# Performance work log

Measured on AMD Instinct MI355X. Metric: run time of the kernel, lower is better.

Reference implementation:

```python
import jax, jax.numpy as jnp
import numpy as np
import math

Ds = 2048
N = 16384
M = 1024


def setup_inputs() -> dict:
    key = jax.random.key(0)
    kD, kS, kW = jax.random.split(key, 3)
    D = jax.random.normal(kD, (N, Ds), dtype=jnp.float32)
    S = jax.random.normal(kS, (M, Ds), dtype=jnp.float32)
    W = jax.random.normal(kW, (Ds, Ds), dtype=jnp.float32) * 0.01  # init.normal std=0.01
    return {"D": D, "S": S, "W": W}


def reference(D, S, W):
    ds = D.shape[1]
    temperature = 1.0
    # cross-attention: [n, m]
    scores = (D @ S.T) / (math.sqrt(ds) * temperature)
    att_weight = jax.nn.softmax(scores, axis=1)
    att_S = att_weight @ S  # [n, Ds]
    # bilinear per row: logits[i] = D[i] . (W @ att_S[i])  -> fused einsum
    logits = jnp.einsum('nd,de,ne->n', D, W, att_S)
    log_prob = jnp.sum(jax.nn.log_sigmoid(logits))
    return log_prob
```

## Files before the change

### kernel.cpp

```cpp
#include <hip/hip_runtime.h>
#include <stdint.h>

typedef unsigned short u16;
typedef unsigned int u32;
typedef __attribute__((ext_vector_type(8))) short bf16x8;
typedef __attribute__((ext_vector_type(4))) float f32x4;

#define DS 2048
#define NROWS 16384
#define MS 1024
#define K2 2048

__device__ __forceinline__ u16 f2bf(float f) {
  u32 u = __float_as_uint(f);
  u32 r = (u + 0x7fffu + ((u >> 16) & 1u)) >> 16;
  return (u16)r;
}
__device__ __forceinline__ float bf2f(u16 h) {
  return __uint_as_float(((u32)h) << 16);
}

__global__ __launch_bounds__(256) void k_conv(const float* __restrict__ in,
                                              u16* __restrict__ out, int n4) {
  int i = blockIdx.x * blockDim.x + threadIdx.x;
  int stride = gridDim.x * blockDim.x;
  for (; i < n4; i += stride) {
    float4 v = ((const float4*)in)[i];
    ushort4 o;
    o.x = f2bf(v.x); o.y = f2bf(v.y); o.z = f2bf(v.z); o.w = f2bf(v.w);
    ((ushort4*)out)[i] = o;
  }
}

__global__ __launch_bounds__(256) void k_conv_S(const float* __restrict__ in,
                                                u16* __restrict__ Sbf,
                                                u16* __restrict__ Bt, int n4) {
  int i = blockIdx.x * blockDim.x + threadIdx.x;
  int stride = gridDim.x * blockDim.x;
  for (; i < n4; i += stride) {
    float4 v = ((const float4*)in)[i];
    ushort4 o;
    o.x = f2bf(v.x); o.y = f2bf(v.y); o.z = f2bf(v.z); o.w = f2bf(v.w);
    ((ushort4*)Sbf)[i] = o;
    int m = i >> 9;
    int c4 = i & 511;
    ((ushort4*)Bt)[(size_t)m * 1024 + c4] = o;
  }
}

__device__ __forceinline__ void gload16(const u16* g, u16* l) {
  __builtin_amdgcn_global_load_lds(
      (const __attribute__((address_space(1))) void*)g,
      (__attribute__((address_space(3))) void*)l, 16, 0, 0);
}

__global__ __launch_bounds__(256, 2) void k_gemm_bt64(const u16* __restrict__ A,
                                                      const u16* __restrict__ Bt,
                                                      u16* __restrict__ C, int ldc,
                                                      int K) {
  __shared__ u16 lsA[64 * 32];
  __shared__ u16 lsB[128 * 32];
  const int tid = threadIdx.x;
  const int wid = tid >> 6;
  const int lane = tid & 63;
  const int brow = blockIdx.y * 64;
  const int bcol = blockIdx.x * 128;
  const int wm = wid >> 1;
  const int wn = wid & 1;

  f32x4 acc[2][4];
#pragma unroll
  for (int i = 0; i < 2; ++i)
#pragma unroll
    for (int j = 0; j < 4; ++j) acc[i][j] = (f32x4){0.f, 0.f, 0.f, 0.f};

  const int srow = lane >> 2;
  const int skoct = (lane & 3) * 8;
  const u16* gA = A + (size_t)(brow + wid * 16 + srow) * K + skoct;
  const u16* gB = Bt + (size_t)(bcol + wid * 32 + srow) * K + skoct;
  u16* lA = &lsA[(wid * 16) * 32];
  u16* lB0 = &lsB[(wid * 32) * 32];
  u16* lB1 = &lsB[(wid * 32 + 16) * 32];
  const size_t row16 = (size_t)16 * K;

  const int arow = wm * 32 + (lane & 15);
  const int bcr = wn * 64 + (lane & 15);
  const int koff = (lane >> 4) * 8;

  for (int kt = 0; kt < K; kt += 32) {
    gload16(gA + kt, lA);
    gload16(gB + kt, lB0);
    gload16(gB + kt + row16, lB1);
    __syncthreads();
    bf16x8 af[2], bfr[4];
#pragma unroll
    for (int i = 0; i < 2; ++i) af[i] = *(const bf16x8*)&lsA[(arow + i * 16) * 32 + koff];
#pragma unroll
    for (int i = 0; i < 4; ++i) bfr[i] = *(const bf16x8*)&lsB[(bcr + i * 16) * 32 + koff];
#pragma unroll
    for (int mi = 0; mi < 2; ++mi)
#pragma unroll
      for (int ni = 0; ni < 4; ++ni)
        acc[mi][ni] = __builtin_amdgcn_mfma_f32_16x16x32_bf16(af[mi], bfr[ni],
                                                              acc[mi][ni], 0, 0, 0);
    __syncthreads();
  }

  const int crow0 = brow + wm * 32 + (lane >> 4) * 4;
  const int ccol0 = bcol + wn * 64 + (lane & 15);
#pragma unroll
  for (int mi = 0; mi < 2; ++mi)
#pragma unroll
    for (int ni = 0; ni < 4; ++ni)
#pragma unroll
      for (int r = 0; r < 4; ++r)
        C[(size_t)(crow0 + mi * 16 + r) * ldc + (ccol0 + ni * 16)] = f2bf(acc[mi][ni][r]);
}

#define SINV 0.022097086912079608f

#define DSR(d, a, IMM) \
  asm volatile("ds_read_b128 %0, %1 offset:%c2" : "=v"(d) : "v"(a), "n"(IMM))

#define RD_A0(k0, k1, dst)                              \
  DSR(dst[0][0], k0, 0);     DSR(dst[0][1], k1, 0);     \
  DSR(dst[1][0], k0, 2048);  DSR(dst[1][1], k1, 2048);  \
  DSR(dst[2][0], k0, 4096);  DSR(dst[2][1], k1, 4096);  \
  DSR(dst[3][0], k0, 6144);  DSR(dst[3][1], k1, 6144)
#define RD_A1(k0, k1, dst)                              \
  DSR(dst[0][0], k0, 16384); DSR(dst[0][1], k1, 16384); \
  DSR(dst[1][0], k0, 18432); DSR(dst[1][1], k1, 18432); \
  DSR(dst[2][0], k0, 20480); DSR(dst[2][1], k1, 20480); \
  DSR(dst[3][0], k0, 22528); DSR(dst[3][1], k1, 22528)
#define RD_B0(k0, k1, dst)                              \
  DSR(dst[0][0], k0, 0);     DSR(dst[0][1], k1, 0);     \
  DSR(dst[1][0], k0, 2048);  DSR(dst[1][1], k1, 2048)
#define RD_B1(k0, k1, dst)                              \
  DSR(dst[0][0], k0, 16384); DSR(dst[0][1], k1, 16384); \
  DSR(dst[1][0], k0, 18432); DSR(dst[1][1], k1, 18432)

#define MMAQ(AF, BQ, QM, QN)                                                       \
  do {                                                                             \
    _Pragma("unroll") for (int mi = 0; mi < 4; ++mi)                               \
        _Pragma("unroll") for (int ni = 0; ni < 2; ++ni) {                         \
      acc[QM][QN][mi][ni] = __builtin_amdgcn_mfma_f32_16x16x32_bf16(               \
          AF[mi][0], BQ[ni][0], acc[QM][QN][mi][ni], 0, 0, 0);                     \
      acc[QM][QN][mi][ni] = __builtin_amdgcn_mfma_f32_16x16x32_bf16(               \
          AF[mi][1], BQ[ni][1], acc[QM][QN][mi][ni], 0, 0, 0);                     \
    }                                                                              \
  } while (0)

#define LGKM(N)                                              \
  asm volatile("s_waitcnt lgkmcnt(" #N ")" ::: "memory");    \
  __builtin_amdgcn_sched_barrier(0)
#define VMW(N) asm volatile("s_waitcnt vmcnt(" #N ")" ::: "memory")
#define PRIO1() __builtin_amdgcn_s_setprio(1)
#define PRIO0() __builtin_amdgcn_s_setprio(0)
#define BAR() __builtin_amdgcn_s_barrier()

#define STGA(b, h, kt)                                                            \
  do {                                                                            \
    gload16(pA + (size_t)((h) * 128) * K2 + (kt),                                 \
            &lds[(b) * 32768 + (h) * 8192 + wid * 512]);                          \
    gload16(pA + (size_t)((h) * 128 + 64) * K2 + (kt),                            \
            &lds[(b) * 32768 + (h) * 8192 + 4096 + wid * 512]);                   \
  } while (0)
#define STGB(b, h, kt)                                                            \
  do {                                                                            \
    gload16(pB + (size_t)((h) * 128) * K2 + (kt),                                 \
            &lds[(b) * 32768 + 16384 + (h) * 8192 + wid * 512]);                  \
    gload16(pB + (size_t)((h) * 128 + 64) * K2 + (kt),                            \
            &lds[(b) * 32768 + 16384 + (h) * 8192 + 4096 + wid * 512]);           \
  } while (0)

__global__ __launch_bounds__(512, 2) void k_gemm8(const u16* __restrict__ A,
                                                  const u16* __restrict__ Bt,
                                                  float* __restrict__ Pnd) {
  extern __shared__ u16 lds[];
  const int tid = threadIdx.x;
  const int wid = tid >> 6;
  const int lane = tid & 63;
  const int bid = blockIdx.x;
  const int swz = (bid & 7) * 64 + (bid >> 3);
  const int by = swz >> 3, bx = swz & 7;
  const int brow = by * 256, bcol = bx * 256;
  const int wm = wid >> 2, wn = wid & 3;
  const int l15 = lane & 15, s0 = lane >> 4;

  const int tr = tid >> 3;
  const int scol = ((tid & 7) ^ (tr & 7)) << 3;
  const u16* pA = A + (size_t)(brow + tr) * K2 + scol;
  const u16* pB = Bt + (size_t)(bcol + tr) * K2 + scol;

  const u32 lb = (u32)(uintptr_t)(&lds[0]);
  const u32 xorp = ((u32)(s0 ^ (lane & 7))) << 4;
  const u32 aA00 = lb + ((u32)(wm * 64 + l15) << 7) + xorp;
  const u32 aA01 = aA00 ^ 64u;
  const u32 aA10 = aA00 + 65536u;
  const u32 aA11 = aA10 ^ 64u;
  const u32 aB00 = lb + 32768u + ((u32)(wn * 32 + l15) << 7) + xorp;
  const u32 aB01 = aB00 ^ 64u;
  const u32 aB10 = aB00 + 65536u;
  const u32 aB11 = aB10 ^ 64u;

  f32x4 acc[2][2][4][2];
#pragma unroll
  for (int a = 0; a < 2; ++a)
#pragma unroll
    for (int b = 0; b < 2; ++b)
#pragma unroll
      for (int c = 0; c < 4; ++c)
#pragma unroll
        for (int d = 0; d < 2; ++d) acc[a][b][c][d] = (f32x4){0.f, 0.f, 0.f, 0.f};

  bf16x8 afA[4][2], afB[4][2], bq0[2][2], bq1[2][2];

  STGA(0, 0, 0); STGB(0, 0, 0); STGB(0, 1, 0); STGA(0, 1, 0);
  STGA(1, 0, 64);
  VMW(2);
  BAR();
  RD_A0(aA00, aA01, afA);
  RD_B0(aB00, aB01, bq0);

  int kb = 0;
#pragma unroll 1
  for (int j = 0; j < 15; ++j, kb += 128) {
    STGB(1, 0, kb + 64);
    RD_B1(aB00, aB01, bq1);
    LGKM(4); PRIO1(); MMAQ(afA, bq0, 0, 0); PRIO0(); VMW(4); BAR();
    STGB(1, 1, kb + 64);
    RD_A1(aA00, aA01, afB);
    LGKM(8); PRIO1(); MMAQ(afA, bq1, 0, 1); PRIO0(); VMW(4); BAR();
    STGA(1, 1, kb + 64);
    LGKM(0); PRIO1(); MMAQ(afB, bq0, 1, 0); PRIO0(); VMW(4); BAR();
    STGA(0, 0, kb + 128);
    RD_A0(aA10, aA11, afA);
    RD_B0(aB10, aB11, bq0);
    LGKM(12); PRIO1(); MMAQ(afB, bq1, 1, 1); PRIO0(); VMW(4); BAR();
    STGB(0, 0, kb + 128);
    RD_B1(aB10, aB11, bq1);
    LGKM(4); PRIO1(); MMAQ(afA, bq0, 0, 0); PRIO0(); VMW(4); BAR();
    STGB(0, 1, kb + 128);
    RD_A1(aA10, aA11, afB);
    LGKM(8); PRIO1(); MMAQ(afA, bq1, 0, 1); PRIO0(); VMW(4); BAR();
    STGA(0, 1, kb + 128);
    LGKM(0); PRIO1(); MMAQ(afB, bq0, 1, 0); PRIO0(); VMW(4); BAR();
    STGA(1, 0, kb + 192);
    RD_A0(aA00, aA01, afA);
    RD_B0(aB00, aB01, bq0);
    LGKM(12); PRIO1(); MMAQ(afB, bq1, 1, 1); PRIO0(); VMW(4); BAR();
  }
  {
    STGB(1, 0, kb + 64);
    RD_B1(aB00, aB01, bq1);
    LGKM(4); PRIO1(); MMAQ(afA, bq0, 0, 0); PRIO0(); VMW(4); BAR();
    STGB(1, 1, kb + 64);
    RD_A1(aA00, aA01, afB);
    LGKM(8); PRIO1(); MMAQ(afA, bq1, 0, 1); PRIO0(); VMW(4); BAR();
    STGA(1, 1, kb + 64);
    LGKM(0); PRIO1(); MMAQ(afB, bq0, 1, 0); PRIO0(); VMW(4); BAR();
    RD_A0(aA10, aA11, afA);
    RD_B0(aB10, aB11, bq0);
    LGKM(12); PRIO1(); MMAQ(afB, bq1, 1, 1); PRIO0(); VMW(2); BAR();
    RD_B1(aB10, aB11, bq1);
    LGKM(4); PRIO1(); MMAQ(afA, bq0, 0, 0); PRIO0(); VMW(0); BAR();
    RD_A1(aA10, aA11, afB);
    LGKM(8); PRIO1(); MMAQ(afA, bq1, 0, 1); PRIO0();
    LGKM(0); PRIO1(); MMAQ(afB, bq0, 1, 0); PRIO0();
    MMAQ(afB, bq1, 1, 1);
  }

  __syncthreads();
  float* red = (float*)&lds[0];

#pragma unroll
  for (int qm = 0; qm < 2; ++qm)
#pragma unroll
    for (int mi = 0; mi < 4; ++mi)
#pragma unroll
      for (int r = 0; r < 4; ++r) {
        float num = 0.f, den = 0.f;
#pragma unroll
        for (int qn = 0; qn < 2; ++qn)
#pragma unroll
          for (int ni = 0; ni < 2; ++ni) {
            float v = acc[qm][qn][mi][ni][r];
            float g = __shfl_xor(v, 1);
            float e = __expf(v * SINV);
            num += e * g;
            den += e;
          }
        num += __shfl_xor(num, 2); den += __shfl_xor(den, 2);
        num += __shfl_xor(num, 4); den += __shfl_xor(den, 4);
        num += __shfl_xor(num, 8); den += __shfl_xor(den, 8);
        if (l15 == 0) {
          int slot = qm * 16 + mi * 4 + r;
          red[((wid * 32 + slot) * 4 + s0) * 2 + 0] = num;
          red[((wid * 32 + slot) * 4 + s0) * 2 + 1] = den;
        }
      }
  __syncthreads();
  {
    int rloc = tid >> 1, which = tid & 1;
    int qm = rloc >> 7, wmr = (rloc >> 6) & 1, mi = (rloc >> 4) & 3;
    int lg = (rloc >> 2) & 3, r = rloc & 3;
    int slot = qm * 16 + mi * 4 + r;
    float v = 0.f;
#pragma unroll
    for (int w2 = 0; w2 < 4; ++w2)
      v += red[(((wmr * 4 + w2) * 32 + slot) * 4 + lg) * 2 + which];
    Pnd[((size_t)(brow + rloc) * 8 + bx) * 2 + which] = v;
  }
}

__global__ __launch_bounds__(256) void k_rowfinal(const float* __restrict__ Pnd,
                                                  float* __restrict__ part) {
  int row = blockIdx.x * 256 + threadIdx.x;
  const float4* p = (const float4*)(Pnd + (size_t)row * 16);
  float num = 0.f, den = 0.f;
#pragma unroll
  for (int i = 0; i < 4; ++i) {
    float4 v = p[i];
    num += v.x + v.z;
    den += v.y + v.w;
  }
  float logit = num / den;
  float ls = (logit >= 0.f) ? -log1pf(__expf(-logit))
                            : (logit - log1pf(__expf(logit)));
  __shared__ float red[4];
#pragma unroll
  for (int off = 32; off > 0; off >>= 1) ls += __shfl_down(ls, off);
  if ((threadIdx.x & 63) == 0) red[threadIdx.x >> 6] = ls;
  __syncthreads();
  if (threadIdx.x == 0) part[blockIdx.x] = red[0] + red[1] + red[2] + red[3];
}

__global__ __launch_bounds__(64) void k_final64(const float* __restrict__ part,
                                                float* __restrict__ out) {
  float v = part[threadIdx.x];
#pragma unroll
  for (int off = 32; off > 0; off >>= 1) v += __shfl_down(v, off);
  if (threadIdx.x == 0) out[0] = v;
}

extern "C" void kernel_launch(void* const* d_in, const int* in_sizes, int n_in,
                              void* d_out, int out_size, void* d_ws, size_t ws_size,
                              hipStream_t stream) {
  const float* D = (const float*)d_in[0];
  const float* S = (const float*)d_in[1];
  const float* W = (const float*)d_in[2];

  char* w = (char*)d_ws;
  u16* Dbf = (u16*)w; w += (size_t)NROWS * DS * 2;
  u16* Bt = (u16*)w;  w += (size_t)DS * DS * 2;
  u16* Wbf = (u16*)w; w += (size_t)DS * DS * 2;
  u16* Sbf = (u16*)w; w += (size_t)MS * DS * 2;
  float* Pnd = (float*)w; w += (size_t)NROWS * 16 * 4;
  float* part = (float*)w;

  (void)hipFuncSetAttribute((const void*)k_gemm8,
                            hipFuncAttributeMaxDynamicSharedMemorySize, 131072);

  k_conv<<<1024, 256, 0, stream>>>(W, Wbf, DS * DS / 4);
  k_conv_S<<<512, 256, 0, stream>>>(S, Sbf, Bt, MS * DS / 4);
  k_conv<<<2048, 256, 0, stream>>>(D, Dbf, NROWS * DS / 4);

  k_gemm_bt64<<<dim3(DS / 128, MS / 64), 256, 0, stream>>>(
      Sbf, Wbf, Bt + DS, 2 * DS, DS);

  k_gemm8<<<512, 512, 131072, stream>>>(Dbf, Bt, Pnd);

  k_rowfinal<<<NROWS / 256, 256, 0, stream>>>(Pnd, part);
  k_final64<<<1, 64, 0, stream>>>(part, (float*)d_out);
}
```

Baseline: 188.7 us.

## Restructure GEMM main loop into four phases with merged MFMA groups

```diff
diff --git a/kernel.cpp b/kernel.cpp
--- a/kernel.cpp
+++ b/kernel.cpp
@@ -154,6 +154,7 @@
   asm volatile("s_waitcnt lgkmcnt(" #N ")" ::: "memory");    \
   __builtin_amdgcn_sched_barrier(0)
 #define VMW(N) asm volatile("s_waitcnt vmcnt(" #N ")" ::: "memory")
+#define SB0() __builtin_amdgcn_sched_barrier(0)
 #define PRIO1() __builtin_amdgcn_s_setprio(1)
 #define PRIO0() __builtin_amdgcn_s_setprio(0)
 #define BAR() __builtin_amdgcn_s_barrier()
@@ -172,6 +173,7 @@
     gload16(pB + (size_t)((h) * 128 + 64) * K2 + (kt),                            \
             &lds[(b) * 32768 + 16384 + (h) * 8192 + 4096 + wid * 512]);           \
   } while (0)
+#define STGB4(b, kt) do { STGB(b, 0, kt); STGB(b, 1, kt); } while (0)
 
 __global__ __launch_bounds__(512, 2) void k_gemm8(const u16* __restrict__ A,
                                                   const u16* __restrict__ Bt,
@@ -215,59 +217,71 @@
 
   bf16x8 afA[4][2], afB[4][2], bq0[2][2], bq1[2][2];
 
-  STGA(0, 0, 0); STGB(0, 0, 0); STGB(0, 1, 0); STGA(0, 1, 0);
+  STGA(0, 0, 0); STGA(0, 1, 0); STGB4(0, 0);
   STGA(1, 0, 64);
   VMW(2);
   BAR();
   RD_A0(aA00, aA01, afA);
   RD_B0(aB00, aB01, bq0);
+  RD_B1(aB00, aB01, bq1);
+  STGB4(1, 64);
 
   int kb = 0;
 #pragma unroll 1
   for (int j = 0; j < 15; ++j, kb += 128) {
-    STGB(1, 0, kb + 64);
+    RD_A1(aA00, aA01, afB);
+    LGKM(8);
+    PRIO1(); MMAQ(afA, bq0, 0, 0); MMAQ(afA, bq1, 0, 1); PRIO0();
+    SB0();
+    STGA(1, 1, kb + 64);
+    STGA(0, 0, kb + 128);
+    VMW(4); BAR();
+    RD_A0(aA10, aA11, afA);
+    LGKM(8);
+    PRIO1(); MMAQ(afB, bq0, 1, 0); MMAQ(afB, bq1, 1, 1); PRIO0();
+    SB0();
+    RD_B0(aB10, aB11, bq0);
+    RD_B1(aB10, aB11, bq1);
+    STGB4(0, kb + 128);
+    VMW(4); BAR();
+    RD_A1(aA10, aA11, afB);
+    LGKM(8);
+    PRIO1(); MMAQ(afA, bq0, 0, 0); MMAQ(afA, bq1, 0, 1); PRIO0();
+    SB0();
+    STGA(0, 1, kb + 128);
+    STGA(1, 0, kb + 192);
+    VMW(4); BAR();
+    RD_A0(aA00, aA01, afA);
+    LGKM(8);
+    PRIO1(); MMAQ(afB, bq0, 1, 0); MMAQ(afB, bq1, 1, 1); PRIO0();
+    SB0();
+    RD_B0(aB00, aB01, bq0);
     RD_B1(aB00, aB01, bq1);
-    LGKM(4); PRIO1(); MMAQ(afA, bq0, 0, 0); PRIO0(); VMW(4); BAR();
-    STGB(1, 1, kb + 64);
+    STGB4(1, kb + 192);
+    VMW(4); BAR();
+  }
+  {
     RD_A1(aA00, aA01, afB);
-    LGKM(8); PRIO1(); MMAQ(afA, bq1, 0, 1); PRIO0(); VMW(4); BAR();
+    LGKM(8);
+    PRIO1(); MMAQ(afA, bq0, 0, 0); MMAQ(afA, bq1, 0, 1); PRIO0();
+    SB0();
     STGA(1, 1, kb + 64);
-    LGKM(0); PRIO1(); MMAQ(afB, bq0, 1, 0); PRIO0(); VMW(4); BAR();
-    STGA(0, 0, kb + 128);
+    VMW(2);
+    BAR();
     RD_A0(aA10, aA11, afA);
+    LGKM(8);
+    PRIO1(); MMAQ(afB, bq0, 1, 0); MMAQ(afB, bq1, 1, 1); PRIO0();
+    SB0();
     RD_B0(aB10, aB11, bq0);
-    LGKM(12); PRIO1(); MMAQ(afB, bq1, 1, 1); PRIO0(); VMW(4); BAR();
-    STGB(0, 0, kb + 128);
     RD_B1(aB10, aB11, bq1);
-    LGKM(4); PRIO1(); MMAQ(afA, bq0, 0, 0); PRIO0(); VMW(4); BAR();
-    STGB(0, 1, kb + 128);
+    VMW(0);
+    BAR();
     RD_A1(aA10, aA11, afB);
-    LGKM(8); PRIO1(); MMAQ(afA, bq1, 0, 1); PRIO0(); VMW(4); BAR();
-    STGA(0, 1, kb + 128);
-    LGKM(0); PRIO1(); MMAQ(afB, bq0, 1, 0); PRIO0(); VMW(4); BAR();
-    STGA(1, 0, kb + 192);
-    RD_A0(aA00, aA01, afA);
-    RD_B0(aB00, aB01, bq0);
-    LGKM(12); PRIO1(); MMAQ(afB, bq1, 1, 1); PRIO0(); VMW(4); BAR();
-  }
-  {
-    STGB(1, 0, kb + 64);
-    RD_B1(aB00, aB01, bq1);
-    LGKM(4); PRIO1(); MMAQ(afA, bq0, 0, 0); PRIO0(); VMW(4); BAR();
-    STGB(1, 1, kb + 64);
-    RD_A1(aA00, aA01, afB);
-    LGKM(8); PRIO1(); MMAQ(afA, bq1, 0, 1); PRIO0(); VMW(4); BAR();
-    STGA(1, 1, kb + 64);
-    LGKM(0); PRIO1(); MMAQ(afB, bq0, 1, 0); PRIO0(); VMW(4); BAR();
-    RD_A0(aA10, aA11, afA);
-    RD_B0(aB10, aB11, bq0);
-    LGKM(12); PRIO1(); MMAQ(afB, bq1, 1, 1); PRIO0(); VMW(2); BAR();
-    RD_B1(aB10, aB11, bq1);
-    LGKM(4); PRIO1(); MMAQ(afA, bq0, 0, 0); PRIO0(); VMW(0); BAR();
-    RD_A1(aA10, aA11, afB);
-    LGKM(8); PRIO1(); MMAQ(afA, bq1, 0, 1); PRIO0();
-    LGKM(0); PRIO1(); MMAQ(afB, bq0, 1, 0); PRIO0();
-    MMAQ(afB, bq1, 1, 1);
+    LGKM(8);
+    PRIO1(); MMAQ(afA, bq0, 0, 0); MMAQ(afA, bq1, 0, 1); PRIO0();
+    SB0();
+    LGKM(0);
+    PRIO1(); MMAQ(afB, bq0, 1, 0); MMAQ(afB, bq1, 1, 1); PRIO0();
   }
 
   __syncthreads();
```

After: 201.0 us. +6.5%, slower.

## Fuse D fp32-to-bf16 conversion into main GEMM A-tile loads

Applied to the files above, without the earlier changes.

```diff
diff --git a/kernel.cpp b/kernel.cpp
--- a/kernel.cpp
+++ b/kernel.cpp
@@ -5,6 +5,7 @@
 typedef unsigned int u32;
 typedef __attribute__((ext_vector_type(8))) short bf16x8;
 typedef __attribute__((ext_vector_type(4))) float f32x4;
+typedef __attribute__((ext_vector_type(4))) u32 u32x4;
 
 #define DS 2048
 #define NROWS 16384
@@ -121,6 +122,10 @@
 
 #define DSR(d, a, IMM) \
   asm volatile("ds_read_b128 %0, %1 offset:%c2" : "=v"(d) : "v"(a), "n"(IMM))
+#define GLD4o(d, a, IMM) \
+  asm volatile("global_load_dwordx4 %0, %1, off offset:%c2" : "=v"(d) : "v"(a), "n"(IMM))
+#define CVTPK(d, lo, hi) \
+  asm("v_cvt_pk_bf16_f32 %0, %1, %2" : "=v"(d) : "v"(lo), "v"(hi))
 
 #define RD_A0(k0, k1, dst)                              \
   DSR(dst[0][0], k0, 0);     DSR(dst[0][1], k1, 0);     \
@@ -154,17 +159,11 @@
   asm volatile("s_waitcnt lgkmcnt(" #N ")" ::: "memory");    \
   __builtin_amdgcn_sched_barrier(0)
 #define VMW(N) asm volatile("s_waitcnt vmcnt(" #N ")" ::: "memory")
+#define SB0() __builtin_amdgcn_sched_barrier(0)
 #define PRIO1() __builtin_amdgcn_s_setprio(1)
 #define PRIO0() __builtin_amdgcn_s_setprio(0)
 #define BAR() __builtin_amdgcn_s_barrier()
 
-#define STGA(b, h, kt)                                                            \
-  do {                                                                            \
-    gload16(pA + (size_t)((h) * 128) * K2 + (kt),                                 \
-            &lds[(b) * 32768 + (h) * 8192 + wid * 512]);                          \
-    gload16(pA + (size_t)((h) * 128 + 64) * K2 + (kt),                            \
-            &lds[(b) * 32768 + (h) * 8192 + 4096 + wid * 512]);                   \
-  } while (0)
 #define STGB(b, h, kt)                                                            \
   do {                                                                            \
     gload16(pB + (size_t)((h) * 128) * K2 + (kt),                                 \
@@ -173,7 +172,27 @@
             &lds[(b) * 32768 + 16384 + (h) * 8192 + 4096 + wid * 512]);           \
   } while (0)
 
-__global__ __launch_bounds__(512, 2) void k_gemm8(const u16* __restrict__ A,
+#define ALOAD(R, h, kt)                                                           \
+  do {                                                                            \
+    const float* _p0 = pAf + (size_t)((h) * 128) * 2048 + (kt);                   \
+    const float* _p1 = _p0 + (size_t)64 * 2048;                                   \
+    GLD4o(R[0], _p0, 0); GLD4o(R[1], _p0, 16);                                    \
+    GLD4o(R[2], _p1, 0); GLD4o(R[3], _p1, 16);                                    \
+  } while (0)
+#define AWRITE(R, b, h)                                                           \
+  do {                                                                            \
+    u32 c0, c1, c2, c3, c4, c5, c6, c7;                                           \
+    CVTPK(c0, R[0][0], R[0][1]); CVTPK(c1, R[0][2], R[0][3]);                     \
+    CVTPK(c2, R[1][0], R[1][1]); CVTPK(c3, R[1][2], R[1][3]);                     \
+    CVTPK(c4, R[2][0], R[2][1]); CVTPK(c5, R[2][2], R[2][3]);                     \
+    CVTPK(c6, R[3][0], R[3][1]); CVTPK(c7, R[3][2], R[3][3]);                     \
+    u32x4 Q0 = {c0, c1, c2, c3}, Q1 = {c4, c5, c6, c7};                           \
+    u32 wa = wbase + (b)*65536u + (h)*16384u;                                     \
+    asm volatile("ds_write_b128 %0, %1" ::"v"(wa), "v"(Q0));                      \
+    asm volatile("ds_write_b128 %0, %1 offset:8192" ::"v"(wa), "v"(Q1));          \
+  } while (0)
+
+__global__ __launch_bounds__(512, 2) void k_gemm8(const float* __restrict__ Af,
                                                   const u16* __restrict__ Bt,
                                                   float* __restrict__ Pnd) {
   extern __shared__ u16 lds[];
@@ -189,10 +208,11 @@
 
   const int tr = tid >> 3;
   const int scol = ((tid & 7) ^ (tr & 7)) << 3;
-  const u16* pA = A + (size_t)(brow + tr) * K2 + scol;
+  const float* pAf = Af + (size_t)(brow + tr) * 2048 + scol;
   const u16* pB = Bt + (size_t)(bcol + tr) * K2 + scol;
 
   const u32 lb = (u32)(uintptr_t)(&lds[0]);
+  const u32 wbase = lb + (u32)wid * 1024u + (u32)(lane * 16);
   const u32 xorp = ((u32)(s0 ^ (lane & 7))) << 4;
   const u32 aA00 = lb + ((u32)(wm * 64 + l15) << 7) + xorp;
   const u32 aA01 = aA00 ^ 64u;
@@ -214,10 +234,13 @@
         for (int d = 0; d < 2; ++d) acc[a][b][c][d] = (f32x4){0.f, 0.f, 0.f, 0.f};
 
   bf16x8 afA[4][2], afB[4][2], bq0[2][2], bq1[2][2];
-
-  STGA(0, 0, 0); STGB(0, 0, 0); STGB(0, 1, 0); STGA(0, 1, 0);
-  STGA(1, 0, 64);
-  VMW(2);
+  f32x4 ra0[4], ra1[4];
+
+  STGB(0, 0, 0); STGB(0, 1, 0);
+  ALOAD(ra0, 0, 0);  VMW(0); SB0(); AWRITE(ra0, 0, 0);
+  ALOAD(ra0, 1, 0);  VMW(0); SB0(); AWRITE(ra0, 0, 1);
+  ALOAD(ra0, 0, 64); VMW(0); SB0(); AWRITE(ra0, 1, 0);
+  LGKM(0);
   BAR();
   RD_A0(aA00, aA01, afA);
   RD_B0(aB00, aB01, bq0);
@@ -226,48 +249,55 @@
 #pragma unroll 1
   for (int j = 0; j < 15; ++j, kb += 128) {
     STGB(1, 0, kb + 64);
+    ALOAD(ra0, 1, kb + 64);
     RD_B1(aB00, aB01, bq1);
-    LGKM(4); PRIO1(); MMAQ(afA, bq0, 0, 0); PRIO0(); VMW(4); BAR();
+    LGKM(4); PRIO1(); MMAQ(afA, bq0, 0, 0); PRIO0(); BAR();
+    STGB(1, 1, kb + 64);
+    ALOAD(ra1, 0, kb + 128);
+    RD_A1(aA00, aA01, afB);
+    LGKM(8); PRIO1(); MMAQ(afA, bq1, 0, 1); PRIO0(); BAR();
+    LGKM(0); PRIO1(); MMAQ(afB, bq0, 1, 0); PRIO0();
+    VMW(6); SB0(); AWRITE(ra0, 1, 1); BAR();
+    VMW(0); SB0();
+    RD_A0(aA10, aA11, afA);
+    RD_B0(aB10, aB11, bq0);
+    LGKM(12); PRIO1(); MMAQ(afB, bq1, 1, 1); PRIO0();
+    AWRITE(ra1, 0, 0); BAR();
+    STGB(0, 0, kb + 128);
+    ALOAD(ra0, 1, kb + 128);
+    RD_B1(aB10, aB11, bq1);
+    LGKM(4); PRIO1(); MMAQ(afA, bq0, 0, 0); PRIO0(); BAR();
+    STGB(0, 1, kb + 128);
+    ALOAD(ra1, 0, kb + 192);
+    RD_A1(aA10, aA11, afB);
+    LGKM(8); PRIO1(); MMAQ(afA, bq1, 0, 1); PRIO0(); BAR();
+    LGKM(0); PRIO1(); MMAQ(afB, bq0, 1, 0); PRIO0();
+    VMW(6); SB0(); AWRITE(ra0, 0, 1); BAR();
+    VMW(0); SB0();
+    RD_A0(aA00, aA01, afA);
+    RD_B0(aB00, aB01, bq0);
+    LGKM(12); PRIO1(); MMAQ(afB, bq1, 1, 1); PRIO0();
+    AWRITE(ra1, 1, 0); BAR();
+  }
+  {
+    STGB(1, 0, kb + 64);
+    ALOAD(ra0, 1, kb + 64);
+    RD_B1(aB00, aB01, bq1);
+    LGKM(4); PRIO1(); MMAQ(afA, bq0, 0, 0); PRIO0(); BAR();
     STGB(1, 1, kb + 64);
     RD_A1(aA00, aA01, afB);
-    LGKM(8); PRIO1(); MMAQ(afA, bq1, 0, 1); PRIO0(); VMW(4); BAR();
-    STGA(1, 1, kb + 64);
-    LGKM(0); PRIO1(); MMAQ(afB, bq0, 1, 0); PRIO0(); VMW(4); BAR();
-    STGA(0, 0, kb + 128);
+    LGKM(8); PRIO1(); MMAQ(afA, bq1, 0, 1); PRIO0(); BAR();
+    LGKM(0); PRIO1(); MMAQ(afB, bq0, 1, 0); PRIO0();
+    VMW(2); SB0(); AWRITE(ra0, 1, 1); BAR();
+    VMW(0); SB0();
     RD_A0(aA10, aA11, afA);
     RD_B0(aB10, aB11, bq0);
-    LGKM(12); PRIO1(); MMAQ(afB, bq1, 1, 1); PRIO0(); VMW(4); BAR();
-    STGB(0, 0, kb + 128);
+    LGKM(12); PRIO1(); MMAQ(afB, bq1, 1, 1); PRIO0(); BAR();
     RD_B1(aB10, aB11, bq1);
-    LGKM(4); PRIO1(); MMAQ(afA, bq0, 0, 0); PRIO0(); VMW(4); BAR();
-    STGB(0, 1, kb + 128);
-    RD_A1(aA10, aA11, afB);
-    LGKM(8); PRIO1(); MMAQ(afA, bq1, 0, 1); PRIO0(); VMW(4); BAR();
-    STGA(0, 1, kb + 128);
-    LGKM(0); PRIO1(); MMAQ(afB, bq0, 1, 0); PRIO0(); VMW(4); BAR();
-    STGA(1, 0, kb + 192);
-    RD_A0(aA00, aA01, afA);
-    RD_B0(aB00, aB01, bq0);
-    LGKM(12); PRIO1(); MMAQ(afB, bq1, 1, 1); PRIO0(); VMW(4); BAR();
-  }
-  {
-    STGB(1, 0, kb + 64);
-    RD_B1(aB00, aB01, bq1);
-    LGKM(4); PRIO1(); MMAQ(afA, bq0, 0, 0); PRIO0(); VMW(4); BAR();
-    STGB(1, 1, kb + 64);
-    RD_A1(aA00, aA01, afB);
-    LGKM(8); PRIO1(); MMAQ(afA, bq1, 0, 1); PRIO0(); VMW(4); BAR();
-    STGA(1, 1, kb + 64);
-    LGKM(0); PRIO1(); MMAQ(afB, bq0, 1, 0); PRIO0(); VMW(4); BAR();
-    RD_A0(aA10, aA11, afA);
-    RD_B0(aB10, aB11, bq0);
-    LGKM(12); PRIO1(); MMAQ(afB, bq1, 1, 1); PRIO0(); VMW(2); BAR();
-    RD_B1(aB10, aB11, bq1);
-    LGKM(4); PRIO1(); MMAQ(afA, bq0, 0, 0); PRIO0(); VMW(0); BAR();
+    LGKM(4); PRIO1(); MMAQ(afA, bq0, 0, 0); PRIO0();
     RD_A1(aA10, aA11, afB);
     LGKM(8); PRIO1(); MMAQ(afA, bq1, 0, 1); PRIO0();
-    LGKM(0); PRIO1(); MMAQ(afB, bq0, 1, 0); PRIO0();
-    MMAQ(afB, bq1, 1, 1);
+    LGKM(0); PRIO1(); MMAQ(afB, bq0, 1, 0); MMAQ(afB, bq1, 1, 1); PRIO0();
   }
 
   __syncthreads();
@@ -351,7 +381,6 @@
   const float* W = (const float*)d_in[2];
 
   char* w = (char*)d_ws;
-  u16* Dbf = (u16*)w; w += (size_t)NROWS * DS * 2;
   u16* Bt = (u16*)w;  w += (size_t)DS * DS * 2;
   u16* Wbf = (u16*)w; w += (size_t)DS * DS * 2;
   u16* Sbf = (u16*)w; w += (size_t)MS * DS * 2;
@@ -363,12 +392,11 @@
 
   k_conv<<<1024, 256, 0, stream>>>(W, Wbf, DS * DS / 4);
   k_conv_S<<<512, 256, 0, stream>>>(S, Sbf, Bt, MS * DS / 4);
-  k_conv<<<2048, 256, 0, stream>>>(D, Dbf, NROWS * DS / 4);
 
   k_gemm_bt64<<<dim3(DS / 128, MS / 64), 256, 0, stream>>>(
       Sbf, Wbf, Bt + DS, 2 * DS, DS);
 
-  k_gemm8<<<512, 512, 131072, stream>>>(Dbf, Bt, Pnd);
+  k_gemm8<<<512, 512, 131072, stream>>>(D, Bt, Pnd);
 
   k_rowfinal<<<NROWS / 256, 256, 0, stream>>>(Pnd, part);
   k_final64<<<1, 64, 0, stream>>>(part, (float*)d_out);
```

New measurement: 350.7 us. +85.8%, slower.

## Double-buffer S·W GEMM LDS loads and merge W/S conversion kernels

Applied to the files above, without the earlier changes.

```diff
diff --git a/kernel.cpp b/kernel.cpp
--- a/kernel.cpp
+++ b/kernel.cpp
@@ -18,6 +18,31 @@
 }
 __device__ __forceinline__ float bf2f(u16 h) {
   return __uint_as_float(((u32)h) << 16);
+}
+
+#define NW4 (DS * DS / 4)
+#define NS4 (MS * DS / 4)
+__global__ __launch_bounds__(256) void k_conv_WS(const float* __restrict__ W,
+                                                 const float* __restrict__ S,
+                                                 u16* __restrict__ Wbf,
+                                                 u16* __restrict__ Sbf,
+                                                 u16* __restrict__ Bt) {
+  int i = blockIdx.x * 256 + threadIdx.x;
+  if (i < NW4) {
+    float4 v = ((const float4*)W)[i];
+    ushort4 o;
+    o.x = f2bf(v.x); o.y = f2bf(v.y); o.z = f2bf(v.z); o.w = f2bf(v.w);
+    ((ushort4*)Wbf)[i] = o;
+  } else {
+    int j = i - NW4;
+    float4 v = ((const float4*)S)[j];
+    ushort4 o;
+    o.x = f2bf(v.x); o.y = f2bf(v.y); o.z = f2bf(v.z); o.w = f2bf(v.w);
+    ((ushort4*)Sbf)[j] = o;
+    int m = j >> 9;
+    int c4 = j & 511;
+    ((ushort4*)Bt)[(size_t)m * 1024 + c4] = o;
+  }
 }
 
 __global__ __launch_bounds__(256) void k_conv(const float* __restrict__ in,
@@ -32,34 +57,23 @@
   }
 }
 
-__global__ __launch_bounds__(256) void k_conv_S(const float* __restrict__ in,
-                                                u16* __restrict__ Sbf,
-                                                u16* __restrict__ Bt, int n4) {
-  int i = blockIdx.x * blockDim.x + threadIdx.x;
-  int stride = gridDim.x * blockDim.x;
-  for (; i < n4; i += stride) {
-    float4 v = ((const float4*)in)[i];
-    ushort4 o;
-    o.x = f2bf(v.x); o.y = f2bf(v.y); o.z = f2bf(v.z); o.w = f2bf(v.w);
-    ((ushort4*)Sbf)[i] = o;
-    int m = i >> 9;
-    int c4 = i & 511;
-    ((ushort4*)Bt)[(size_t)m * 1024 + c4] = o;
-  }
-}
-
 __device__ __forceinline__ void gload16(const u16* g, u16* l) {
   __builtin_amdgcn_global_load_lds(
       (const __attribute__((address_space(1))) void*)g,
       (__attribute__((address_space(3))) void*)l, 16, 0, 0);
 }
 
+#define VMW3() asm volatile("s_waitcnt vmcnt(3)" ::: "memory")
+#define VMW0f() asm volatile("s_waitcnt vmcnt(0)" ::: "memory")
+#define RBAR() __builtin_amdgcn_s_barrier()
+#define RSB0() __builtin_amdgcn_sched_barrier(0)
+
 __global__ __launch_bounds__(256, 2) void k_gemm_bt64(const u16* __restrict__ A,
                                                       const u16* __restrict__ Bt,
                                                       u16* __restrict__ C, int ldc,
                                                       int K) {
-  __shared__ u16 lsA[64 * 32];
-  __shared__ u16 lsB[128 * 32];
+  __shared__ u16 lsA[2][64 * 32];
+  __shared__ u16 lsB[2][128 * 32];
   const int tid = threadIdx.x;
   const int wid = tid >> 6;
   const int lane = tid & 63;
@@ -78,33 +92,48 @@
   const int skoct = (lane & 3) * 8;
   const u16* gA = A + (size_t)(brow + wid * 16 + srow) * K + skoct;
   const u16* gB = Bt + (size_t)(bcol + wid * 32 + srow) * K + skoct;
-  u16* lA = &lsA[(wid * 16) * 32];
-  u16* lB0 = &lsB[(wid * 32) * 32];
-  u16* lB1 = &lsB[(wid * 32 + 16) * 32];
   const size_t row16 = (size_t)16 * K;
 
   const int arow = wm * 32 + (lane & 15);
   const int bcr = wn * 64 + (lane & 15);
   const int koff = (lane >> 4) * 8;
 
-  for (int kt = 0; kt < K; kt += 32) {
-    gload16(gA + kt, lA);
-    gload16(gB + kt, lB0);
-    gload16(gB + kt + row16, lB1);
-    __syncthreads();
+#define VSTG(b, kt)                                        \
+  do {                                                     \
+    gload16(gA + (kt), &lsA[b][(wid * 16) * 32]);          \
+    gload16(gB + (kt), &lsB[b][(wid * 32) * 32]);          \
+    gload16(gB + (kt) + row16, &lsB[b][(wid * 32 + 16) * 32]); \
+  } while (0)
+
+  VSTG(0, 0);
+  const int NT = K / 32;
+#pragma unroll 1
+  for (int t = 0; t < NT; ++t) {
+    const int b = t & 1;
+    if (t < NT - 1) {
+      VSTG(b ^ 1, (t + 1) * 32);
+      VMW3();
+    } else {
+      VMW0f();
+    }
+    RBAR(); RSB0();
     bf16x8 af[2], bfr[4];
 #pragma unroll
-    for (int i = 0; i < 2; ++i) af[i] = *(const bf16x8*)&lsA[(arow + i * 16) * 32 + koff];
-#pragma unroll
-    for (int i = 0; i < 4; ++i) bfr[i] = *(const bf16x8*)&lsB[(bcr + i * 16) * 32 + koff];
+    for (int i = 0; i < 2; ++i)
+      af[i] = *(const bf16x8*)&lsA[b][(arow + i * 16) * 32 + koff];
+#pragma unroll
+    for (int i = 0; i < 4; ++i)
+      bfr[i] = *(const bf16x8*)&lsB[b][(bcr + i * 16) * 32 + koff];
 #pragma unroll
     for (int mi = 0; mi < 2; ++mi)
 #pragma unroll
       for (int ni = 0; ni < 4; ++ni)
         acc[mi][ni] = __builtin_amdgcn_mfma_f32_16x16x32_bf16(af[mi], bfr[ni],
                                                               acc[mi][ni], 0, 0, 0);
-    __syncthreads();
-  }
+    RSB0();
+    RBAR();
+  }
+#undef VSTG
 
   const int crow0 = brow + wm * 32 + (lane >> 4) * 4;
   const int ccol0 = bcol + wn * 64 + (lane & 15);
@@ -361,8 +390,7 @@
   (void)hipFuncSetAttribute((const void*)k_gemm8,
                             hipFuncAttributeMaxDynamicSharedMemorySize, 131072);
 
-  k_conv<<<1024, 256, 0, stream>>>(W, Wbf, DS * DS / 4);
-  k_conv_S<<<512, 256, 0, stream>>>(S, Sbf, Bt, MS * DS / 4);
+  k_conv_WS<<<(NW4 + NS4) / 256, 256, 0, stream>>>(W, S, Wbf, Sbf, Bt);
   k_conv<<<2048, 256, 0, stream>>>(D, Dbf, NROWS * DS / 4);
 
   k_gemm_bt64<<<dim3(DS / 128, MS / 64), 256, 0, stream>>>(
```

After: 190.6 us. Within noise of the previous version (+1.0%).
